# Kernel tuning notes

Hardware: AMD Instinct MI355X
Metric: run time of the kernel (lower is better)

## Reference

```python
import jax, jax.numpy as jnp
import numpy as np

DIM = 256
RATIO = 4
SCALE = 8
B, H, W = 16, 128, 128
EPS = 1e-5


def _conv(x, w, pad):
    return jax.lax.conv_general_dilated(
        x, w, window_strides=(1, 1), padding=[(pad, pad), (pad, pad)],
        dimension_numbers=('NCHW', 'OIHW', 'NCHW'))


def _haar_dwt(x):
    # pywt.dwt2(x, 'haar') on even-sized inputs == strided 2x2 sum/difference
    a = x[:, :, 0::2, 0::2]
    b = x[:, :, 0::2, 1::2]
    c = x[:, :, 1::2, 0::2]
    d = x[:, :, 1::2, 1::2]
    ll = (a + b + c + d) * 0.5
    lh = (a + b - c - d) * 0.5  # cH: high-pass along rows
    hl = (a - b + c - d) * 0.5  # cV: high-pass along cols
    hh = (a - b - c + d) * 0.5  # cD
    return jnp.concatenate([ll, lh, hl, hh], axis=1)


def setup_inputs() -> dict:
    key = jax.random.key(0)
    ks = jax.random.split(key, 16)
    dq = DIM // RATIO
    ds = DIM // SCALE
    s = 0.05
    return {
        'x': jax.random.normal(ks[0], (B, DIM, H, W), jnp.float32),
        'reduce_w': jax.random.normal(ks[1], (dq, DIM, 1, 1), jnp.float32) * s,
        'reduce_b': jnp.zeros((dq,), jnp.float32),
        'bn_g': jnp.ones((dq,), jnp.float32),
        'bn_b': jnp.zeros((dq,), jnp.float32),
        'bn_mean': jnp.zeros((dq,), jnp.float32),
        'bn_var': jnp.ones((dq,), jnp.float32),
        'conv_w': jax.random.normal(ks[2], (1, DIM, 1, 1), jnp.float32) * s,
        'conv1_w': jax.random.normal(ks[3], (DIM, DIM, 1, 1), jnp.float32) * s,
        'conv2_w': jax.random.normal(ks[4], (DIM, DIM, 3, 3), jnp.float32) * s,
        'conv3_w': jax.random.normal(ks[5], (DIM, DIM, 5, 5), jnp.float32) * s,
        'conv4_w': jax.random.normal(ks[6], (DIM, DIM, 7, 7), jnp.float32) * s,
        'channel_conv_w': jax.random.normal(ks[7], (DIM, DIM, 3, 3), jnp.float32) * s,
        'conv1x1_w': jax.random.normal(ks[8], (DIM, 6 * DIM, 3, 3), jnp.float32) * s,
        'ct1_w': jax.random.normal(ks[9], (ds, DIM, 1, 1), jnp.float32) * s,
        'ct1_b': jnp.zeros((ds,), jnp.float32),
        'ln_g': jnp.ones((ds,), jnp.float32),
        'ln_b': jnp.zeros((ds,), jnp.float32),
        'ct2_w': jax.random.normal(ks[10], (DIM, ds, 1, 1), jnp.float32) * s,
        'ct2_b': jnp.zeros((DIM,), jnp.float32),
        'proj_w': jax.random.normal(ks[11], (DIM, DIM, 1, 1), jnp.float32) * s,
    }


def reference(x, reduce_w, reduce_b, bn_g, bn_b, bn_mean, bn_var, conv_w,
              conv1_w, conv2_w, conv3_w, conv4_w, channel_conv_w, conv1x1_w,
              ct1_w, ct1_b, ln_g, ln_b, ct2_w, ct2_b, proj_w):
    # max-pool 2x2 stride 2
    p = jax.lax.reduce_window(x, -jnp.inf, jax.lax.max,
                              (1, 1, 2, 2), (1, 1, 2, 2), 'VALID')
    # reduce: 1x1 conv -> BN (inference) -> ReLU
    r = _conv(x, reduce_w, 0) + reduce_b[None, :, None, None]
    r = (r - bn_mean[None, :, None, None]) * jax.lax.rsqrt(bn_var + EPS)[None, :, None, None]
    r = jax.nn.relu(r * bn_g[None, :, None, None] + bn_b[None, :, None, None])
    # Haar DWT (original runs under no_grad: detached from autograd)
    qkv0 = jax.lax.stop_gradient(_haar_dwt(r))  # [B, DIM, H/2, W/2]
    qkv1 = _conv(qkv0, conv1_w, 0)
    qkv2 = _conv(qkv0, conv2_w, 1)
    qkv3 = _conv(qkv0, conv3_w, 2)
    qkv4 = _conv(qkv0, conv4_w, 3)
    qkv = _conv(jnp.concatenate([qkv0, qkv1, qkv2, qkv3, qkv4, p], axis=1),
                conv1x1_w, 1)  # [B, DIM, H/2, W/2]
    n = (H // 2) * (W // 2)
    # spatial attention weights: softmax over spatial positions
    content = _conv(qkv, conv_w, 0).reshape(B, n)          # [B, N]
    content = jax.nn.softmax(content, axis=1)
    channel = _conv(qkv, channel_conv_w, 1).reshape(B, DIM, n)  # [B, C, N]
    pooled = jnp.einsum('bcn,bn->bc', channel, content)[:, :, None, None]
    # channel transform: 1x1 -> LayerNorm over (C,1,1) -> ReLU -> 1x1
    t = _conv(pooled, ct1_w, 0) + ct1_b[None, :, None, None]
    mu = jnp.mean(t, axis=(1, 2, 3), keepdims=True)
    var = jnp.mean(jnp.square(t - mu), axis=(1, 2, 3), keepdims=True)
    t = (t - mu) * jax.lax.rsqrt(var + EPS)
    t = jax.nn.relu(t * ln_g[None, :, None, None] + ln_b[None, :, None, None])
    cw = _conv(t, ct2_w, 0) + ct2_b[None, :, None, None]  # [B, DIM, 1, 1]
    return _conv(qkv * cw, proj_w, 0)
```

## Files before the change

### kernel.cpp

```cpp
#include <hip/hip_runtime.h>
#include <stdint.h>


typedef __attribute__((ext_vector_type(8))) short bf16x8;
typedef __attribute__((ext_vector_type(4))) float f32x4;

#define EPS_ 1e-5f

#define GLOAD16(gp, lp)                                                        \
  __builtin_amdgcn_global_load_lds(                                            \
      (const __attribute__((address_space(1))) void*)(gp),                     \
      (__attribute__((address_space(3))) void*)(lp), 16, 0, 0)

__device__ __forceinline__ float bf2f(unsigned short u) {
  union { unsigned int u; float f; } c; c.u = ((unsigned int)u) << 16; return c.f;
}
__device__ __forceinline__ unsigned short f2bf(float f) {
  union { float f; unsigned int u; } c; c.f = f;
  return (unsigned short)((c.u + 0x7fffu + ((c.u >> 16) & 1u)) >> 16);
}
__device__ __forceinline__ void unpack8(uint4 v, float* f) {
  f[0]=bf2f((unsigned short)(v.x&0xffffu)); f[1]=bf2f((unsigned short)(v.x>>16));
  f[2]=bf2f((unsigned short)(v.y&0xffffu)); f[3]=bf2f((unsigned short)(v.y>>16));
  f[4]=bf2f((unsigned short)(v.z&0xffffu)); f[5]=bf2f((unsigned short)(v.z>>16));
  f[6]=bf2f((unsigned short)(v.w&0xffffu)); f[7]=bf2f((unsigned short)(v.w>>16));
}
__device__ __forceinline__ uint4 pack8(const float* f) {
  uint4 v;
  v.x = (unsigned)f2bf(f[0]) | ((unsigned)f2bf(f[1])<<16);
  v.y = (unsigned)f2bf(f[2]) | ((unsigned)f2bf(f[3])<<16);
  v.z = (unsigned)f2bf(f[4]) | ((unsigned)f2bf(f[5])<<16);
  v.w = (unsigned)f2bf(f[6]) | ((unsigned)f2bf(f[7])<<16);
  return v;
}

__global__ void k_repack(const float* __restrict__ src, unsigned short* __restrict__ dst,
                         int O, int Opad, int I, int T) {
  int gid = blockIdx.x * 256 + threadIdx.x;
  if (gid >= Opad * I * T) return;
  int i = gid % I; int r = gid / I; int o = r % Opad; int t = r / Opad;
  dst[gid] = (o < O) ? f2bf(src[((size_t)(o * I + i)) * T + t]) : (unsigned short)0;
}

__global__ void k_border_zero(unsigned short* __restrict__ buf, int PW, int PB, int C) {
  int IW = PW - 2 * PB;
  int nb = PW * PW - IW * IW;
  int per = C >> 3;
  int gid = blockIdx.x * 256 + threadIdx.x;
  if (gid >= 16 * nb * per) return;
  int cq = gid % per; int r = gid / per; int p = r % nb; int b = r / nb;
  int y, x;
  int top = PB * PW;
  if (p < top) { y = p / PW; x = p - y * PW; }
  else if (p < top + IW * 2 * PB) {
    int q = p - top; y = PB + q / (2 * PB); int rr = q % (2 * PB);
    x = (rr < PB) ? rr : (IW + rr);
  } else { int q = p - top - IW * 2 * PB; y = PB + IW + q / PW; x = q - (q / PW) * PW; }
  uint4 z; z.x = z.y = z.z = z.w = 0u;
  *(uint4*)&buf[(((size_t)b * PW + y) * PW + x) * C + cq * 8] = z;
}

__global__ void k_transpose_x(const float* __restrict__ x, unsigned short* __restrict__ xh) {
  int by = blockIdx.x; int b = by >> 7; int y = by & 127;
  int tid = threadIdx.x;
  __shared__ unsigned short lds[32 * 129];
  for (int c0 = 0; c0 < 256; c0 += 32) {
    #pragma unroll
    for (int i = 0; i < 16; ++i) {
      int e = i * 256 + tid; int ci = e >> 7, xx = e & 127;
      float v = x[(((size_t)b * 256 + c0 + ci) * 128 + y) * 128 + xx];
      lds[ci * 129 + xx] = f2bf(v);
    }
    __syncthreads();
    #pragma unroll
    for (int i2 = 0; i2 < 2; ++i2) {
      int e = i2 * 256 + tid; int pix = e >> 2, q = e & 3;
      unsigned int w0, w1, w2, w3;
      w0 = (unsigned)lds[(q*8+0)*129 + pix] | ((unsigned)lds[(q*8+1)*129 + pix] << 16);
      w1 = (unsigned)lds[(q*8+2)*129 + pix] | ((unsigned)lds[(q*8+3)*129 + pix] << 16);
      w2 = (unsigned)lds[(q*8+4)*129 + pix] | ((unsigned)lds[(q*8+5)*129 + pix] << 16);
      w3 = (unsigned)lds[(q*8+6)*129 + pix] | ((unsigned)lds[(q*8+7)*129 + pix] << 16);
      uint4 v; v.x = w0; v.y = w1; v.z = w2; v.w = w3;
      *(uint4*)&xh[(((size_t)b * 128 + y) * 128 + pix) * 256 + c0 + q * 8] = v;
    }
    __syncthreads();
  }
}

__global__ void k_maxpool(const unsigned short* __restrict__ xh, unsigned short* __restrict__ cat) {
  int gid = blockIdx.x * 256 + threadIdx.x;
  int cq = gid & 31; int pix = gid >> 5;
  int bb = pix >> 12; int yx = pix & 4095;
  int y = yx >> 6, xx2 = yx & 63;
  size_t base = (((size_t)bb * 128 + 2 * y) * 128 + 2 * xx2) * 256 + cq * 8;
  uint4 v00 = *(const uint4*)(xh + base);
  uint4 v01 = *(const uint4*)(xh + base + 256);
  uint4 v10 = *(const uint4*)(xh + base + 32768);
  uint4 v11 = *(const uint4*)(xh + base + 32768 + 256);
  float a[8], b8[8], c8[8], d8[8], m8[8];
  unpack8(v00, a); unpack8(v01, b8); unpack8(v10, c8); unpack8(v11, d8);
  #pragma unroll
  for (int j = 0; j < 8; ++j) m8[j] = fmaxf(fmaxf(a[j], b8[j]), fmaxf(c8[j], d8[j]));
  *(uint4*)(cat + (((size_t)bb * 4900 + (y + 3) * 70 + (xx2 + 3))) * 1536 + 1280 + cq * 8) = pack8(m8);
}

__global__ void k_haar(const unsigned short* __restrict__ rbn, unsigned short* __restrict__ cat) {
  int gid = blockIdx.x * 256 + threadIdx.x;
  int cq = gid & 7; int pix = gid >> 3;
  int bb = pix >> 12; int yx = pix & 4095;
  int y = yx >> 6, xx = yx & 63;
  size_t base = (((size_t)bb * 128 + 2 * y) * 128 + 2 * xx) * 64 + cq * 8;
  uint4 va = *(const uint4*)(rbn + base);
  uint4 vb = *(const uint4*)(rbn + base + 64);
  uint4 vc = *(const uint4*)(rbn + base + 8192);
  uint4 vd = *(const uint4*)(rbn + base + 8192 + 64);
  float a[8], b8[8], c8[8], d8[8], o[8];
  unpack8(va, a); unpack8(vb, b8); unpack8(vc, c8); unpack8(vd, d8);
  size_t ob = ((size_t)bb * 4900 + (y + 3) * 70 + (xx + 3)) * 1536 + cq * 8;
  #pragma unroll
  for (int j = 0; j < 8; ++j) o[j] = (a[j] + b8[j] + c8[j] + d8[j]) * 0.5f;
  *(uint4*)(cat + ob + 0)   = pack8(o);
  #pragma unroll
  for (int j = 0; j < 8; ++j) o[j] = (a[j] + b8[j] - c8[j] - d8[j]) * 0.5f;
  *(uint4*)(cat + ob + 64)  = pack8(o);
  #pragma unroll
  for (int j = 0; j < 8; ++j) o[j] = (a[j] - b8[j] + c8[j] - d8[j]) * 0.5f;
  *(uint4*)(cat + ob + 128) = pack8(o);
  #pragma unroll
  for (int j = 0; j < 8; ++j) o[j] = (a[j] - b8[j] - c8[j] + d8[j]) * 0.5f;
  *(uint4*)(cat + ob + 192) = pack8(o);
}

__global__ __launch_bounds__(512, 2) void k_conv_gemm256(
    const unsigned short* __restrict__ Wt, const unsigned short* __restrict__ Bf,
    int Cin, int Cstr, int cbase,
    int PW, int PB, int KH, int pad,
    unsigned long long wbstride,
    unsigned short* __restrict__ outb, int OCstr, int ocbase, int OPW, int OPB,
    float* __restrict__ outf, int mode) {
  const int tid = threadIdx.x, lane = tid & 63, w = tid >> 6;
  const int wm = w >> 2, wn = w & 3;
  const int bn = blockIdx.x * 256;
  const int b = blockIdx.z;
  if (wbstride) Wt += (size_t)b * wbstride;
  extern __shared__ unsigned short S[];

  f32x4 zero4 = {0.f, 0.f, 0.f, 0.f};
  f32x4 acc[8][4];
  #pragma unroll
  for (int i = 0; i < 8; ++i)
    #pragma unroll
    for (int j = 0; j < 4; ++j) acc[i][j] = zero4;

  const int srow = lane >> 3;
  const int csrc = ((lane & 7) - srow) & 7;
  const size_t jA = (size_t)8 * Cin;
  const unsigned short* aSt = Wt + ((size_t)(w * 32 + srow)) * Cin + csrc * 8;
  const size_t bimg = (size_t)b * PW * PW;
  const unsigned short* bSt[4];
  #pragma unroll
  for (int j = 0; j < 4; ++j) {
    int p = bn + w * 32 + j * 8 + srow;
    int y = p >> 6, x = p & 63;
    bSt[j] = Bf + (bimg + (size_t)(y + PB) * PW + (x + PB)) * Cstr + cbase + csrc * 8;
  }
  const int dstA = w * 2048;
  const int dstB = 16384 + w * 2048;

  const int r = lane & 15, s4 = lane >> 4;
  const int ck0 = (s4 + (r & 7)) & 7;
  const int dk1 = (ck0 < 4) ? 32 : -32;
  const int aOff = (wm * 128 + r) * 64 + ck0 * 8;
  const int bOff = 16384 + (wn * 64 + r) * 64 + ck0 * 8;

  const size_t MC = (size_t)256 * Cin;
  const int NT = (KH * KH * Cin) >> 6;

  const long long pB0 = ((long long)(0 - pad) * PW + (0 - pad)) * (long long)Cstr;
  #pragma unroll
  for (int j = 0; j < 4; ++j) GLOAD16(aSt + (size_t)j * jA, S + dstA + j * 512);
  #pragma unroll
  for (int j = 0; j < 4; ++j) GLOAD16(bSt[j] + pB0, S + dstB + j * 512);
  __syncthreads();

  int kcn = 0, tyn = 0, txn = 0;
  for (int kt = 0; kt < NT; ++kt) {
    const unsigned short* Sc = S + (kt & 1) * 32768;
    unsigned short* Sn = S + ((kt & 1) ^ 1) * 32768;
    const bool hn = (kt + 1 < NT);
    long long nA = 0, nB = 0;
    if (hn) {
      kcn += 64;
      if (kcn == Cin) { kcn = 0; ++txn; if (txn == KH) { txn = 0; ++tyn; } }
      nA = (long long)(tyn * KH + txn) * MC + kcn;
      nB = ((long long)(tyn - pad) * PW + (txn - pad)) * (long long)Cstr + kcn;
    }
    bf16x8 a[4], bb[4];
    #pragma unroll
    for (int mi = 0; mi < 4; ++mi) a[mi] = *(const bf16x8*)(Sc + aOff + mi * 1024);
    #pragma unroll
    for (int ni = 0; ni < 4; ++ni) bb[ni] = *(const bf16x8*)(Sc + bOff + ni * 1024);
    if (hn) {
      #pragma unroll
      for (int j = 0; j < 4; ++j) GLOAD16(aSt + (size_t)j * jA + nA, Sn + dstA + j * 512);
    }
    __builtin_amdgcn_s_barrier();
    __builtin_amdgcn_s_setprio(1);
    #pragma unroll
    for (int mi = 0; mi < 4; ++mi)
      #pragma unroll
      for (int ni = 0; ni < 4; ++ni)
        acc[mi][ni] = __builtin_amdgcn_mfma_f32_16x16x32_bf16(a[mi], bb[ni], acc[mi][ni], 0, 0, 0);
    __builtin_amdgcn_s_setprio(0);
    __builtin_amdgcn_s_barrier();
    #pragma unroll
    for (int mi = 0; mi < 4; ++mi) a[mi] = *(const bf16x8*)(Sc + aOff + (mi + 4) * 1024);
    if (hn) {
      #pragma unroll
      for (int j = 0; j < 4; ++j) GLOAD16(bSt[j] + nB, Sn + dstB + j * 512);
    }
    __builtin_amdgcn_s_barrier();
    __builtin_amdgcn_s_setprio(1);
    #pragma unroll
    for (int mi = 0; mi < 4; ++mi)
      #pragma unroll
      for (int ni = 0; ni < 4; ++ni)
        acc[mi + 4][ni] = __builtin_amdgcn_mfma_f32_16x16x32_bf16(a[mi], bb[ni], acc[mi + 4][ni], 0, 0, 0);
    __builtin_amdgcn_s_setprio(0);
    __builtin_amdgcn_s_barrier();
    #pragma unroll
    for (int mi = 0; mi < 4; ++mi) a[mi] = *(const bf16x8*)(Sc + aOff + mi * 1024 + dk1);
    #pragma unroll
    for (int ni = 0; ni < 4; ++ni) bb[ni] = *(const bf16x8*)(Sc + bOff + ni * 1024 + dk1);
    __builtin_amdgcn_s_barrier();
    __builtin_amdgcn_s_setprio(1);
    #pragma unroll
    for (int mi = 0; mi < 4; ++mi)
      #pragma unroll
      for (int ni = 0; ni < 4; ++ni)
        acc[mi][ni] = __builtin_amdgcn_mfma_f32_16x16x32_bf16(a[mi], bb[ni], acc[mi][ni], 0, 0, 0);
    __builtin_amdgcn_s_setprio(0);
    __builtin_amdgcn_s_barrier();
    #pragma unroll
    for (int mi = 0; mi < 4; ++mi) a[mi] = *(const bf16x8*)(Sc + aOff + (mi + 4) * 1024 + dk1);
    __builtin_amdgcn_s_barrier();
    __builtin_amdgcn_s_setprio(1);
    #pragma unroll
    for (int mi = 0; mi < 4; ++mi)
      #pragma unroll
      for (int ni = 0; ni < 4; ++ni)
        acc[mi + 4][ni] = __builtin_amdgcn_mfma_f32_16x16x32_bf16(a[mi], bb[ni], acc[mi + 4][ni], 0, 0, 0);
    __builtin_amdgcn_s_setprio(0);
    asm volatile("s_waitcnt vmcnt(0)" ::: "memory");
    __builtin_amdgcn_s_barrier();
  }

  const size_t bimgO = (size_t)b * OPW * OPW;
  #pragma unroll
  for (int mi = 0; mi < 8; ++mi) {
    const int mf = wm * 128 + mi * 16 + (lane >> 4) * 4;
    #pragma unroll
    for (int ni = 0; ni < 4; ++ni) {
      const int n = bn + wn * 64 + ni * 16 + (lane & 15);
      if (mode == 2) {
        #pragma unroll
        for (int vv = 0; vv < 4; ++vv)
          outf[((size_t)b * 256 + mf + vv) * 4096 + n] = acc[mi][ni][vv];
      } else {
        const int oy = n >> 6, ox = n & 63;
        unsigned short h[4];
        #pragma unroll
        for (int vv = 0; vv < 4; ++vv) h[vv] = f2bf(acc[mi][ni][vv]);
        uint2 st; st.x = (unsigned)h[0] | ((unsigned)h[1] << 16);
        st.y = (unsigned)h[2] | ((unsigned)h[3] << 16);
        *(uint2*)&outb[(bimgO + (size_t)(oy + OPB) * OPW + (ox + OPB)) * OCstr + ocbase + mf] = st;
      }
    }
  }
}

__global__ __launch_bounds__(256) void k_conv_gemm(
    const unsigned short* __restrict__ Wt, const unsigned short* __restrict__ Bf,
    int M, int Mpad, int Cin, int Cstr, int cbase,
    int OW, int lgOW, int PW, int PB, int KH, int pad,
    unsigned long long wbstride,
    unsigned short* __restrict__ outb, int OCstr, int ocbase, int OPW, int OPB,
    float* __restrict__ outf, int mode,
    const float* __restrict__ rb, const float* __restrict__ bng, const float* __restrict__ bnb,
    const float* __restrict__ bnm, const float* __restrict__ bnv) {
  const int tid = threadIdx.x, lane = tid & 63, w = tid >> 6;
  const int wm = w >> 1, wn = w & 1;
  const int bm = blockIdx.y * 128, bn = blockIdx.x * 128;
  const int b = blockIdx.z;
  const int Npix = OW * OW;
  if (wbstride) Wt += (size_t)b * wbstride;

  __shared__ __align__(1024) unsigned short sA[128 * 32];
  __shared__ __align__(1024) unsigned short sB[128 * 32];

  f32x4 zero4 = {0.f, 0.f, 0.f, 0.f};
  f32x4 acc[4][4];
  #pragma unroll
  for (int i = 0; i < 4; ++i)
    #pragma unroll
    for (int j = 0; j < 4; ++j) acc[i][j] = zero4;

  const int srow = lane >> 2;
  const int slog = (lane & 3) ^ ((lane >> 3) & 3);
  const int r0 = w * 32;
  const unsigned short* aRow = Wt + ((size_t)(bm + r0 + srow)) * Cin + slog * 8;
  const int n0 = bn + r0 + srow, n1 = n0 + 16;
  const int y0 = n0 >> lgOW, x0 = n0 & (OW - 1);
  const int y1 = n1 >> lgOW, x1 = n1 & (OW - 1);
  const size_t bimg = (size_t)b * PW * PW;
  const unsigned short* bRow0 = Bf + (bimg + (size_t)(y0 + PB) * PW + (x0 + PB)) * Cstr + cbase + slog * 8;
  const unsigned short* bRow1 = Bf + (bimg + (size_t)(y1 + PB) * PW + (x1 + PB)) * Cstr + cbase + slog * 8;
  unsigned short* ldsA0 = &sA[(r0) * 32];
  unsigned short* ldsA1 = &sA[(r0 + 16) * 32];
  unsigned short* ldsB0 = &sB[(r0) * 32];
  unsigned short* ldsB1 = &sB[(r0 + 16) * 32];

  const int rowfrag = lane & 15, hi = lane >> 4;
  const int sl = hi ^ ((rowfrag >> 1) & 3);
  const bf16x8* pA[4]; const bf16x8* pB[4];
  #pragma unroll
  for (int mi = 0; mi < 4; ++mi)
    pA[mi] = (const bf16x8*)&sA[(wm * 64 + mi * 16 + rowfrag) * 32 + sl * 8];
  #pragma unroll
  for (int ni = 0; ni < 4; ++ni)
    pB[ni] = (const bf16x8*)&sB[(wn * 64 + ni * 16 + rowfrag) * 32 + sl * 8];

  const size_t MC = (size_t)Mpad * Cin;
  for (int ty = 0; ty < KH; ++ty) {
    for (int tx = 0; tx < KH; ++tx) {
      const unsigned short* at = aRow + (size_t)(ty * KH + tx) * MC;
      const long long toff = ((long long)(ty - pad) * PW + (tx - pad)) * Cstr;
      const unsigned short* bt0 = bRow0 + toff;
      const unsigned short* bt1 = bRow1 + toff;
      for (int kc = 0; kc < Cin; kc += 32) {
        GLOAD16(at + kc, ldsA0);
        GLOAD16(at + (size_t)16 * Cin + kc, ldsA1);
        GLOAD16(bt0 + kc, ldsB0);
        GLOAD16(bt1 + kc, ldsB1);
        __syncthreads();
        bf16x8 af[4], bfr[4];
        #pragma unroll
        for (int mi = 0; mi < 4; ++mi) af[mi] = *pA[mi];
        #pragma unroll
        for (int ni = 0; ni < 4; ++ni) bfr[ni] = *pB[ni];
        #pragma unroll
        for (int mi = 0; mi < 4; ++mi)
          #pragma unroll
          for (int ni = 0; ni < 4; ++ni)
            acc[mi][ni] = __builtin_amdgcn_mfma_f32_16x16x32_bf16(af[mi], bfr[ni], acc[mi][ni], 0, 0, 0);
        __syncthreads();
      }
    }
  }

  const int mb0 = bm + wm * 64, nb0 = bn + wn * 64;
  const size_t bimgO = (size_t)b * OPW * OPW;
  #pragma unroll
  for (int mi = 0; mi < 4; ++mi) {
    const int mf = mb0 + mi * 16 + (lane >> 4) * 4;
    if (mf >= M) continue;
    #pragma unroll
    for (int ni = 0; ni < 4; ++ni) {
      const int n = nb0 + ni * 16 + (lane & 15);
      if (mode == 2) {
        #pragma unroll
        for (int vv = 0; vv < 4; ++vv)
          outf[((size_t)b * M + mf + vv) * Npix + n] = acc[mi][ni][vv];
      } else {
        const int oy = n >> lgOW, ox = n & (OW - 1);
        unsigned short h[4];
        #pragma unroll
        for (int vv = 0; vv < 4; ++vv) {
          float val = acc[mi][ni][vv];
          if (mode == 1) {
            int m = mf + vv;
            float scl = bng[m] * rsqrtf(bnv[m] + EPS_);
            val = (val + rb[m] - bnm[m]) * scl + bnb[m];
            val = fmaxf(val, 0.f);
          }
          h[vv] = f2bf(val);
        }
        uint2 st; st.x = (unsigned)h[0] | ((unsigned)h[1] << 16);
        st.y = (unsigned)h[2] | ((unsigned)h[3] << 16);
        *(uint2*)&outb[(bimgO + (size_t)(oy + OPB) * OPW + (ox + OPB)) * OCstr + ocbase + mf] = st;
      }
    }
  }
}

__global__ void k_content_logits(const unsigned short* __restrict__ qkv,
                                 const float* __restrict__ conv_w,
                                 float* __restrict__ logits) {
  int j = blockIdx.x, b = blockIdx.y, tid = threadIdx.x;
  __shared__ float wl[256];
  wl[tid] = conv_w[tid];
  __syncthreads();
  int pl = tid >> 3, kp = tid & 7;
  #pragma unroll
  for (int pass = 0; pass < 4; ++pass) {
    int p = j * 128 + pass * 32 + pl;
    int y = p >> 6, x = p & 63;
    const unsigned short* q = qkv + (((size_t)b * 66 + y + 1) * 66 + (x + 1)) * 256 + kp * 32;
    float s = 0.f;
    #pragma unroll
    for (int i = 0; i < 32; i += 8) {
      uint4 v = *(const uint4*)(q + i);
      float f[8]; unpack8(v, f);
      #pragma unroll
      for (int k = 0; k < 8; ++k) s += f[k] * wl[kp * 32 + i + k];
    }
    s += __shfl_down(s, 4, 8);
    s += __shfl_down(s, 2, 8);
    s += __shfl_down(s, 1, 8);
    if (kp == 0) logits[(size_t)b * 4096 + p] = s;
  }
}

__global__ void k_softmax4096(float* __restrict__ cont) {
  int b = blockIdx.x, tid = threadIdx.x;
  __shared__ float red[256];
  float sv[16]; float mx = -1e30f;
  #pragma unroll
  for (int j = 0; j < 16; ++j) { sv[j] = cont[(size_t)b * 4096 + j * 256 + tid]; mx = fmaxf(mx, sv[j]); }
  red[tid] = mx; __syncthreads();
  for (int s = 128; s > 0; s >>= 1) { if (tid < s) red[tid] = fmaxf(red[tid], red[tid + s]); __syncthreads(); }
  mx = red[0]; __syncthreads();
  float sum = 0.f;
  #pragma unroll
  for (int j = 0; j < 16; ++j) { sv[j] = expf(sv[j] - mx); sum += sv[j]; }
  red[tid] = sum; __syncthreads();
  for (int s = 128; s > 0; s >>= 1) { if (tid < s) red[tid] += red[tid + s]; __syncthreads(); }
  float inv = 1.f / red[0];
  #pragma unroll
  for (int j = 0; j < 16; ++j) cont[(size_t)b * 4096 + j * 256 + tid] = sv[j] * inv;
}

__global__ void k_pooled_part(const unsigned short* __restrict__ chn,
                              const float* __restrict__ content, float* __restrict__ ppart) {
  int j = blockIdx.x, b = blockIdx.y, c = threadIdx.x;
  const unsigned short* base = chn + (size_t)b * 4096 * 256 + c;
  const float* ct = content + (size_t)b * 4096;
  float acc = 0.f;
  int n0 = j * 128;
  for (int n = n0; n < n0 + 128; ++n)
    acc += bf2f(base[(size_t)n * 256]) * ct[n];
  ppart[((size_t)b * 32 + j) * 256 + c] = acc;
}
__global__ void k_pooled_red(const float* __restrict__ ppart, float* __restrict__ pooled) {
  int b = blockIdx.x, c = threadIdx.x;
  float s = 0.f;
  #pragma unroll
  for (int j = 0; j < 32; ++j) s += ppart[((size_t)b * 32 + j) * 256 + c];
  pooled[b * 256 + c] = s;
}

__global__ void k_ct(const float* __restrict__ pooled,
                     const float* __restrict__ ct1w, const float* __restrict__ ct1b,
                     const float* __restrict__ lng, const float* __restrict__ lnb,
                     const float* __restrict__ ct2w, const float* __restrict__ ct2b,
                     float* __restrict__ cw) {
  int b = blockIdx.x, tid = threadIdx.x;
  __shared__ float tt[32];
  __shared__ float stats[2];
  if (tid < 32) {
    float s = 0.f;
    const float* w = ct1w + tid * 256;
    const float* p = pooled + b * 256;
    for (int i = 0; i < 256; ++i) s += w[i] * p[i];
    tt[tid] = s + ct1b[tid];
  }
  __syncthreads();
  if (tid == 0) {
    float mu = 0.f;
    for (int j = 0; j < 32; ++j) mu += tt[j];
    mu *= (1.f / 32.f);
    float va = 0.f;
    for (int j = 0; j < 32; ++j) { float d = tt[j] - mu; va += d * d; }
    va *= (1.f / 32.f);
    stats[0] = mu; stats[1] = rsqrtf(va + EPS_);
  }
  __syncthreads();
  if (tid < 32) {
    float v = (tt[tid] - stats[0]) * stats[1];
    tt[tid] = fmaxf(v * lng[tid] + lnb[tid], 0.f);
  }
  __syncthreads();
  float s = 0.f;
  const float* w2 = ct2w + tid * 32;
  #pragma unroll
  for (int j = 0; j < 32; ++j) s += w2[j] * tt[j];
  cw[b * 256 + tid] = s + ct2b[tid];
}

__global__ void k_aproj(const float* __restrict__ projw, const float* __restrict__ cw,
                        unsigned short* __restrict__ aproj) {
  int gid = blockIdx.x * 256 + threadIdx.x;
  int b = gid >> 16; int oi = gid & 65535; int i = oi & 255;
  aproj[gid] = f2bf(projw[oi] * cw[b * 256 + i]);
}

extern "C" void kernel_launch(void* const* d_in, const int* in_sizes, int n_in,
                              void* d_out, int out_size, void* d_ws, size_t ws_size,
                              hipStream_t stream) {
  (void)in_sizes; (void)n_in; (void)out_size; (void)ws_size;
  const float* x        = (const float*)d_in[0];
  const float* reduce_w = (const float*)d_in[1];
  const float* reduce_b = (const float*)d_in[2];
  const float* bn_g     = (const float*)d_in[3];
  const float* bn_b     = (const float*)d_in[4];
  const float* bn_mean  = (const float*)d_in[5];
  const float* bn_var   = (const float*)d_in[6];
  const float* conv_w   = (const float*)d_in[7];
  const float* conv1_w  = (const float*)d_in[8];
  const float* conv2_w  = (const float*)d_in[9];
  const float* conv3_w  = (const float*)d_in[10];
  const float* conv4_w  = (const float*)d_in[11];
  const float* chconv_w = (const float*)d_in[12];
  const float* cat_w    = (const float*)d_in[13];
  const float* ct1_w    = (const float*)d_in[14];
  const float* ct1_b    = (const float*)d_in[15];
  const float* ln_g     = (const float*)d_in[16];
  const float* ln_b     = (const float*)d_in[17];
  const float* ct2_w    = (const float*)d_in[18];
  const float* ct2_b    = (const float*)d_in[19];
  const float* proj_w   = (const float*)d_in[20];

  static bool attr_done = false;
  if (!attr_done) {
    hipFuncSetAttribute(reinterpret_cast<const void*>(&k_conv_gemm256),
                        hipFuncAttributeMaxDynamicSharedMemorySize, 131072);
    attr_done = true;
  }

  char* wsp = (char*)d_ws;
  size_t off = 0;
  auto alloc = [&](size_t bytes) -> char* {
    char* p = wsp + off; off += (bytes + 255) & ~(size_t)255; return p;
  };
  unsigned short* XH    = (unsigned short*)alloc((size_t)16 * 16384 * 256 * 2);
  unsigned short* CAT   = (unsigned short*)alloc((size_t)16 * 4900 * 1536 * 2);
  unsigned short* RBN   = (unsigned short*)alloc((size_t)16 * 16384 * 64 * 2);
  unsigned short* CHN   = RBN;
  unsigned short* QKV   = (unsigned short*)alloc((size_t)16 * 4356 * 256 * 2);
  float*          CONT  = (float*)alloc((size_t)16 * 4096 * 4);
  float*          PPART = (float*)alloc((size_t)16 * 32 * 256 * 4);
  float*          POOL  = (float*)alloc(16 * 256 * 4);
  float*          CWB   = (float*)alloc(16 * 256 * 4);
  unsigned short* WR    = (unsigned short*)alloc((size_t)128 * 256 * 2);
  unsigned short* W1    = (unsigned short*)alloc((size_t)256 * 256 * 2);
  unsigned short* W2    = (unsigned short*)alloc((size_t)9 * 256 * 256 * 2);
  unsigned short* W3    = (unsigned short*)alloc((size_t)25 * 256 * 256 * 2);
  unsigned short* W4    = (unsigned short*)alloc((size_t)49 * 256 * 256 * 2);
  unsigned short* WC    = (unsigned short*)alloc((size_t)9 * 256 * 256 * 2);
  unsigned short* WCAT  = (unsigned short*)alloc((size_t)9 * 256 * 1536 * 2);
  unsigned short* APROJ = (unsigned short*)alloc((size_t)16 * 256 * 256 * 2);

  auto rp = [&](const float* s, unsigned short* d, int O, int Opad, int I, int T) {
    int tot = Opad * I * T;
    k_repack<<<(tot + 255) / 256, 256, 0, stream>>>(s, d, O, Opad, I, T);
  };
  rp(reduce_w, WR, 64, 128, 256, 1);
  rp(conv1_w, W1, 256, 256, 256, 1);
  rp(conv2_w, W2, 256, 256, 256, 9);
  rp(conv3_w, W3, 256, 256, 256, 25);
  rp(conv4_w, W4, 256, 256, 256, 49);
  rp(chconv_w, WC, 256, 256, 256, 9);
  rp(cat_w, WCAT, 256, 256, 1536, 9);

  k_border_zero<<<(16 * 804 * 192 + 255) / 256, 256, 0, stream>>>(CAT, 70, 3, 1536);
  k_border_zero<<<(16 * 260 * 32 + 255) / 256, 256, 0, stream>>>(QKV, 66, 1, 256);

  k_transpose_x<<<2048, 256, 0, stream>>>(x, XH);
  k_maxpool<<<8192, 256, 0, stream>>>(XH, CAT);

  dim3 blk(256);
  dim3 g256(16, 1, 16);
  k_conv_gemm<<<dim3(128, 1, 16), blk, 0, stream>>>(WR, XH, 64, 128, 256, 256, 0,
      128, 7, 128, 0, 1, 0, 0ULL, RBN, 64, 0, 128, 0, nullptr, 1,
      reduce_b, bn_g, bn_b, bn_mean, bn_var);
  k_haar<<<2048, 256, 0, stream>>>(RBN, CAT);
  k_conv_gemm256<<<g256, 512, 131072, stream>>>(W1, CAT, 256, 1536, 0,
      70, 3, 1, 0, 0ULL, CAT, 1536, 256, 70, 3, nullptr, 0);
  k_conv_gemm256<<<g256, 512, 131072, stream>>>(W2, CAT, 256, 1536, 0,
      70, 3, 3, 1, 0ULL, CAT, 1536, 512, 70, 3, nullptr, 0);
  k_conv_gemm256<<<g256, 512, 131072, stream>>>(W3, CAT, 256, 1536, 0,
      70, 3, 5, 2, 0ULL, CAT, 1536, 768, 70, 3, nullptr, 0);
  k_conv_gemm256<<<g256, 512, 131072, stream>>>(W4, CAT, 256, 1536, 0,
      70, 3, 7, 3, 0ULL, CAT, 1536, 1024, 70, 3, nullptr, 0);
  k_conv_gemm256<<<g256, 512, 131072, stream>>>(WCAT, CAT, 1536, 1536, 0,
      70, 3, 3, 1, 0ULL, QKV, 256, 0, 66, 1, nullptr, 0);
  k_content_logits<<<dim3(32, 16), blk, 0, stream>>>(QKV, conv_w, CONT);
  k_softmax4096<<<16, blk, 0, stream>>>(CONT);
  k_conv_gemm256<<<g256, 512, 131072, stream>>>(WC, QKV, 256, 256, 0,
      66, 1, 3, 1, 0ULL, CHN, 256, 0, 64, 0, nullptr, 0);
  k_pooled_part<<<dim3(32, 16), blk, 0, stream>>>(CHN, CONT, PPART);
  k_pooled_red<<<16, blk, 0, stream>>>(PPART, POOL);
  k_ct<<<16, blk, 0, stream>>>(POOL, ct1_w, ct1_b, ln_g, ln_b, ct2_w, ct2_b, CWB);
  k_aproj<<<4096, 256, 0, stream>>>(proj_w, CWB, APROJ);
  k_conv_gemm256<<<g256, 512, 131072, stream>>>(APROJ, QKV, 256, 256, 0,
      66, 1, 1, 0, 65536ULL, nullptr, 256, 0, 64, 0, (float*)d_out, 2);
}
```

Before: 1.451 ms.

## Switch conv GEMM to 4-stage K=32 LDS pipeline with XCD-aware block remap

Rewrites the main implicit-GEMM conv kernel's main loop. It now loads K slices of 32 instead of 64 into a 4-buffer LDS ring with prefetch distance two, and waits with partial vmcnt so loads stay in flight across iterations. This replaces the 2-buffer scheme that drained all loads every iteration, and the barriers inside each iteration are reduced. The grid becomes 1D with a block-index remap that spreads consecutive blocks across XCDs. Launch bounds drop to one block per CU, and the K steps per tile become twice as frequent, which adds loop overhead.

```diff
diff --git a/kernel.cpp b/kernel.cpp
--- a/kernel.cpp
+++ b/kernel.cpp
@@ -131,7 +131,7 @@
   *(uint4*)(cat + ob + 192) = pack8(o);
 }
 
-__global__ __launch_bounds__(512, 2) void k_conv_gemm256(
+__global__ __launch_bounds__(512, 1) void k_conv_gemm256(
     const unsigned short* __restrict__ Wt, const unsigned short* __restrict__ Bf,
     int Cin, int Cstr, int cbase,
     int PW, int PB, int KH, int pad,
@@ -140,8 +140,9 @@
     float* __restrict__ outf, int mode) {
   const int tid = threadIdx.x, lane = tid & 63, w = tid >> 6;
   const int wm = w >> 2, wn = w & 3;
-  const int bn = blockIdx.x * 256;
-  const int b = blockIdx.z;
+  const int nidx = (blockIdx.x & 7) * 32 + (blockIdx.x >> 3);
+  const int bn = (nidx & 15) * 256;
+  const int b = nidx >> 4;
   if (wbstride) Wt += (size_t)b * wbstride;
   extern __shared__ unsigned short S[];
 
@@ -152,59 +153,63 @@
     #pragma unroll
     for (int j = 0; j < 4; ++j) acc[i][j] = zero4;
 
-  const int srow = lane >> 3;
-  const int csrc = ((lane & 7) - srow) & 7;
-  const size_t jA = (size_t)8 * Cin;
-  const unsigned short* aSt = Wt + ((size_t)(w * 32 + srow)) * Cin + csrc * 8;
+  const int srow = lane >> 2, slot = lane & 3;
+  const int csrc = (slot - (srow >> 2)) & 3;
+  const unsigned short* aSt = Wt + (size_t)(w * 32 + srow) * Cin + csrc * 8;
+  const size_t jA = (size_t)16 * Cin;
   const size_t bimg = (size_t)b * PW * PW;
-  const unsigned short* bSt[4];
-  #pragma unroll
-  for (int j = 0; j < 4; ++j) {
-    int p = bn + w * 32 + j * 8 + srow;
-    int y = p >> 6, x = p & 63;
-    bSt[j] = Bf + (bimg + (size_t)(y + PB) * PW + (x + PB)) * Cstr + cbase + csrc * 8;
-  }
-  const int dstA = w * 2048;
-  const int dstB = 16384 + w * 2048;
+  const unsigned short* bSt0; const unsigned short* bSt1;
+  {
+    int p = bn + w * 32 + srow;
+    bSt0 = Bf + (bimg + (size_t)((p >> 6) + PB) * PW + ((p & 63) + PB)) * Cstr + cbase + csrc * 8;
+    p += 16;
+    bSt1 = Bf + (bimg + (size_t)((p >> 6) + PB) * PW + ((p & 63) + PB)) * Cstr + cbase + csrc * 8;
+  }
+  const int dstA0 = w * 1024;
+  const int dstB0 = 8192 + w * 1024;
 
   const int r = lane & 15, s4 = lane >> 4;
-  const int ck0 = (s4 + (r & 7)) & 7;
-  const int dk1 = (ck0 < 4) ? 32 : -32;
-  const int aOff = (wm * 128 + r) * 64 + ck0 * 8;
-  const int bOff = 16384 + (wn * 64 + r) * 64 + ck0 * 8;
+  const int ck = (s4 + (r >> 2)) & 3;
+  const int aOff = (wm * 128 + r) * 32 + ck * 8;
+  const int bOff = 8192 + (wn * 64 + r) * 32 + ck * 8;
 
   const size_t MC = (size_t)256 * Cin;
-  const int NT = (KH * KH * Cin) >> 6;
-
-  const long long pB0 = ((long long)(0 - pad) * PW + (0 - pad)) * (long long)Cstr;
-  #pragma unroll
-  for (int j = 0; j < 4; ++j) GLOAD16(aSt + (size_t)j * jA, S + dstA + j * 512);
-  #pragma unroll
-  for (int j = 0; j < 4; ++j) GLOAD16(bSt[j] + pB0, S + dstB + j * 512);
-  __syncthreads();
-
-  int kcn = 0, tyn = 0, txn = 0;
-  for (int kt = 0; kt < NT; ++kt) {
-    const unsigned short* Sc = S + (kt & 1) * 32768;
-    unsigned short* Sn = S + ((kt & 1) ^ 1) * 32768;
-    const bool hn = (kt + 1 < NT);
-    long long nA = 0, nB = 0;
+  const int NT = (KH * KH * Cin) >> 5;
+
+  const long long t0B = ((long long)(-pad) * PW + (-pad)) * (long long)Cstr;
+  GLOAD16(aSt,             S + dstA0);
+  GLOAD16(aSt + jA,        S + dstA0 + 512);
+  GLOAD16(bSt0 + t0B,      S + dstB0);
+  GLOAD16(bSt1 + t0B,      S + dstB0 + 512);
+  GLOAD16(aSt + 32,        S + 16384 + dstA0);
+  GLOAD16(aSt + jA + 32,   S + 16384 + dstA0 + 512);
+  GLOAD16(bSt0 + t0B + 32, S + 16384 + dstB0);
+  GLOAD16(bSt1 + t0B + 32, S + 16384 + dstB0 + 512);
+  asm volatile("s_waitcnt vmcnt(4)" ::: "memory");
+  __builtin_amdgcn_s_barrier();
+  __builtin_amdgcn_sched_barrier(0);
+
+  int kc2 = 64, ty2 = 0, tx2 = 0;
+  for (int t = 0; t < NT; ++t) {
+    const unsigned short* Sc = S + (t & 3) * 16384;
+    unsigned short* Sn = (unsigned short*)S + ((t + 2) & 3) * 16384;
+    const bool hn = (t + 2) < NT;
+    long long offA = 0, offB = 0;
     if (hn) {
-      kcn += 64;
-      if (kcn == Cin) { kcn = 0; ++txn; if (txn == KH) { txn = 0; ++tyn; } }
-      nA = (long long)(tyn * KH + txn) * MC + kcn;
-      nB = ((long long)(tyn - pad) * PW + (txn - pad)) * (long long)Cstr + kcn;
+      offA = (long long)(ty2 * KH + tx2) * MC + kc2;
+      offB = ((long long)(ty2 - pad) * PW + (tx2 - pad)) * (long long)Cstr + kc2;
+      kc2 += 32;
+      if (kc2 == Cin) { kc2 = 0; ++tx2; if (tx2 == KH) { tx2 = 0; ++ty2; } }
     }
     bf16x8 a[4], bb[4];
     #pragma unroll
-    for (int mi = 0; mi < 4; ++mi) a[mi] = *(const bf16x8*)(Sc + aOff + mi * 1024);
-    #pragma unroll
-    for (int ni = 0; ni < 4; ++ni) bb[ni] = *(const bf16x8*)(Sc + bOff + ni * 1024);
+    for (int mi = 0; mi < 4; ++mi) a[mi] = *(const bf16x8*)(Sc + aOff + mi * 512);
+    #pragma unroll
+    for (int ni = 0; ni < 4; ++ni) bb[ni] = *(const bf16x8*)(Sc + bOff + ni * 512);
     if (hn) {
-      #pragma unroll
-      for (int j = 0; j < 4; ++j) GLOAD16(aSt + (size_t)j * jA + nA, Sn + dstA + j * 512);
-    }
-    __builtin_amdgcn_s_barrier();
+      GLOAD16(aSt + offA,      Sn + dstA0);
+      GLOAD16(aSt + jA + offA, Sn + dstA0 + 512);
+    }
     __builtin_amdgcn_s_setprio(1);
     #pragma unroll
     for (int mi = 0; mi < 4; ++mi)
@@ -214,12 +219,11 @@
     __builtin_amdgcn_s_setprio(0);
     __builtin_amdgcn_s_barrier();
     #pragma unroll
-    for (int mi = 0; mi < 4; ++mi) a[mi] = *(const bf16x8*)(Sc + aOff + (mi + 4) * 1024);
+    for (int mi = 0; mi < 4; ++mi) a[mi] = *(const bf16x8*)(Sc + aOff + (mi + 4) * 512);
     if (hn) {
-      #pragma unroll
-      for (int j = 0; j < 4; ++j) GLOAD16(bSt[j] + nB, Sn + dstB + j * 512);
-    }
-    __builtin_amdgcn_s_barrier();
+      GLOAD16(bSt0 + offB, Sn + dstB0);
+      GLOAD16(bSt1 + offB, Sn + dstB0 + 512);
+    }
     __builtin_amdgcn_s_setprio(1);
     #pragma unroll
     for (int mi = 0; mi < 4; ++mi)
@@ -227,32 +231,12 @@
       for (int ni = 0; ni < 4; ++ni)
         acc[mi + 4][ni] = __builtin_amdgcn_mfma_f32_16x16x32_bf16(a[mi], bb[ni], acc[mi + 4][ni], 0, 0, 0);
     __builtin_amdgcn_s_setprio(0);
-    __builtin_amdgcn_s_barrier();
-    #pragma unroll
-    for (int mi = 0; mi < 4; ++mi) a[mi] = *(const bf16x8*)(Sc + aOff + mi * 1024 + dk1);
-    #pragma unroll
-    for (int ni = 0; ni < 4; ++ni) bb[ni] = *(const bf16x8*)(Sc + bOff + ni * 1024 + dk1);
-    __builtin_amdgcn_s_barrier();
-    __builtin_amdgcn_s_setprio(1);
-    #pragma unroll
-    for (int mi = 0; mi < 4; ++mi)
-      #pragma unroll
-      for (int ni = 0; ni < 4; ++ni)
-        acc[mi][ni] = __builtin_amdgcn_mfma_f32_16x16x32_bf16(a[mi], bb[ni], acc[mi][ni], 0, 0, 0);
-    __builtin_amdgcn_s_setprio(0);
-    __builtin_amdgcn_s_barrier();
-    #pragma unroll
-    for (int mi = 0; mi < 4; ++mi) a[mi] = *(const bf16x8*)(Sc + aOff + (mi + 4) * 1024 + dk1);
-    __builtin_amdgcn_s_barrier();
-    __builtin_amdgcn_s_setprio(1);
-    #pragma unroll
-    for (int mi = 0; mi < 4; ++mi)
-      #pragma unroll
-      for (int ni = 0; ni < 4; ++ni)
-        acc[mi + 4][ni] = __builtin_amdgcn_mfma_f32_16x16x32_bf16(a[mi], bb[ni], acc[mi + 4][ni], 0, 0, 0);
-    __builtin_amdgcn_s_setprio(0);
-    asm volatile("s_waitcnt vmcnt(0)" ::: "memory");
-    __builtin_amdgcn_s_barrier();
+    if (t + 1 < NT) {
+      if (t + 2 < NT) { asm volatile("s_waitcnt vmcnt(4)" ::: "memory"); }
+      else            { asm volatile("s_waitcnt vmcnt(0)" ::: "memory"); }
+      __builtin_amdgcn_s_barrier();
+      __builtin_amdgcn_sched_barrier(0);
+    }
   }
 
   const size_t bimgO = (size_t)b * OPW * OPW;
@@ -579,29 +563,28 @@
   k_maxpool<<<8192, 256, 0, stream>>>(XH, CAT);
 
   dim3 blk(256);
-  dim3 g256(16, 1, 16);
   k_conv_gemm<<<dim3(128, 1, 16), blk, 0, stream>>>(WR, XH, 64, 128, 256, 256, 0,
       128, 7, 128, 0, 1, 0, 0ULL, RBN, 64, 0, 128, 0, nullptr, 1,
       reduce_b, bn_g, bn_b, bn_mean, bn_var);
   k_haar<<<2048, 256, 0, stream>>>(RBN, CAT);
-  k_conv_gemm256<<<g256, 512, 131072, stream>>>(W1, CAT, 256, 1536, 0,
+  k_conv_gemm256<<<256, 512, 131072, stream>>>(W1, CAT, 256, 1536, 0,
       70, 3, 1, 0, 0ULL, CAT, 1536, 256, 70, 3, nullptr, 0);
-  k_conv_gemm256<<<g256, 512, 131072, stream>>>(W2, CAT, 256, 1536, 0,
+  k_conv_gemm256<<<256, 512, 131072, stream>>>(W2, CAT, 256, 1536, 0,
       70, 3, 3, 1, 0ULL, CAT, 1536, 512, 70, 3, nullptr, 0);
-  k_conv_gemm256<<<g256, 512, 131072, stream>>>(W3, CAT, 256, 1536, 0,
+  k_conv_gemm256<<<256, 512, 131072, stream>>>(W3, CAT, 256, 1536, 0,
       70, 3, 5, 2, 0ULL, CAT, 1536, 768, 70, 3, nullptr, 0);
-  k_conv_gemm256<<<g256, 512, 131072, stream>>>(W4, CAT, 256, 1536, 0,
+  k_conv_gemm256<<<256, 512, 131072, stream>>>(W4, CAT, 256, 1536, 0,
       70, 3, 7, 3, 0ULL, CAT, 1536, 1024, 70, 3, nullptr, 0);
-  k_conv_gemm256<<<g256, 512, 131072, stream>>>(WCAT, CAT, 1536, 1536, 0,
+  k_conv_gemm256<<<256, 512, 131072, stream>>>(WCAT, CAT, 1536, 1536, 0,
       70, 3, 3, 1, 0ULL, QKV, 256, 0, 66, 1, nullptr, 0);
   k_content_logits<<<dim3(32, 16), blk, 0, stream>>>(QKV, conv_w, CONT);
   k_softmax4096<<<16, blk, 0, stream>>>(CONT);
-  k_conv_gemm256<<<g256, 512, 131072, stream>>>(WC, QKV, 256, 256, 0,
+  k_conv_gemm256<<<256, 512, 131072, stream>>>(WC, QKV, 256, 256, 0,
       66, 1, 3, 1, 0ULL, CHN, 256, 0, 64, 0, nullptr, 0);
   k_pooled_part<<<dim3(32, 16), blk, 0, stream>>>(CHN, CONT, PPART);
   k_pooled_red<<<16, blk, 0, stream>>>(PPART, POOL);
   k_ct<<<16, blk, 0, stream>>>(POOL, ct1_w, ct1_b, ln_g, ln_b, ct2_w, ct2_b, CWB);
   k_aproj<<<4096, 256, 0, stream>>>(proj_w, CWB, APROJ);
-  k_conv_gemm256<<<g256, 512, 131072, stream>>>(APROJ, QKV, 256, 256, 0,
+  k_conv_gemm256<<<256, 512, 131072, stream>>>(APROJ, QKV, 256, 256, 0,
       66, 1, 1, 0, 65536ULL, nullptr, 256, 0, 64, 0, (float*)d_out, 2);
 }
```

New measurement: 1.474 ms. No clear change (+1.6%).
